# Performance work log

Measured on AMD Instinct MI355X. Metric: run time of the kernel, lower is better.

The kernel has to match this reference:

```python
import jax, jax.numpy as jnp
import numpy as np

MIN_RANGE, MAX_RANGE = 1, 3

def _build_offsets():
    # replicates TorchGrouper.__init__: offsets over a hollow cube neighborhood
    r = np.concatenate([np.arange(-MAX_RANGE, -MIN_RANGE), np.arange(MIN_RANGE, MAX_RANGE)])
    p = r.shape[0]
    rx = np.broadcast_to(r.reshape(1, 1, -1), (p, p, p))
    ry = np.broadcast_to(r.reshape(1, -1, 1), (p, p, p))
    rz = np.broadcast_to(r.reshape(-1, 1, 1), (p, p, p))
    off = np.stack([np.zeros_like(rx), rx, ry, rz], axis=3).reshape(-1, 4)  # [O,4], cols (0,x,y,z)
    return jnp.asarray(off, dtype=jnp.int32)


def setup_inputs() -> dict:
    key = jax.random.key(0)
    k1, k2, k3, k4 = jax.random.split(key, 4)
    N, Z, Y, X = 2, 40, 400, 400
    G, M, C = 40000, 100000, 64
    # voxel map values in [-1, M-1]; -1 == empty voxel (maps to zero feature row)
    voxel_maps = jax.random.randint(k1, (N, Z, Y, X), -1, M, dtype=jnp.int32)
    b = jax.random.randint(k2, (G, 1), 0, N).astype(jnp.float32)
    zyx = jax.random.uniform(k3, (G, 3), dtype=jnp.float32) * jnp.array([Z - 1, Y - 1, X - 1], jnp.float32)
    grid_positions = jnp.concatenate([b, zyx], axis=1)  # [G,4] float (batch,z,y,x)
    features = jax.random.normal(k4, (M, C), dtype=jnp.float32)
    return {"voxel_maps": voxel_maps, "grid_positions": grid_positions, "features": features}


def reference(voxel_maps, grid_positions, features):
    offsets = _build_offsets()                     # [O,4] int32
    O = offsets.shape[0]
    N, Z, Y, X = voxel_maps.shape
    G = grid_positions.shape[0]

    gp_f = grid_positions[:, None, :] + offsets[None].astype(grid_positions.dtype)  # [G,O,4] float
    gp = gp_f.astype(jnp.int32)                    # trunc-toward-zero, matches torch .long()
    bi = gp[..., 0]
    zi = jnp.clip(gp[..., 1], 0, Z - 1)
    yi = jnp.clip(gp[..., 2], 0, Y - 1)
    xi = jnp.clip(gp[..., 3], 0, X - 1)
    sampled_idx = voxel_maps[bi, zi, yi, xi]       # [G,O] int32

    feats_pad = jnp.concatenate([jnp.zeros((1, features.shape[1]), features.dtype), features], axis=0)  # [M+1,C]
    sf = feats_pad[sampled_idx + 1]                # [G,O,C]
    sampled_features = jnp.transpose(sf, (2, 0, 1))[None]  # [1,C,G,O]

    gpf = jnp.transpose(gp_f[..., 1:], (2, 0, 1))[None]    # [1,3,G,O] (z,y,x) coords
    gpf = gpf - jnp.trunc(gpf)                     # fractional part (torch .long().float())
    # faithful quirk: original adds index_offset[:, :3] == columns (0, x, y)
    gpf = gpf + offsets[:, :3].T.astype(gpf.dtype).reshape(1, 3, 1, O)

    empty_mask = jnp.sum(sampled_idx + 1, axis=1) == 0     # [G] bool
    return sampled_features, gpf, empty_mask
```

## Files before the change

### kernel.cpp

```cpp
#include <hip/hip_runtime.h>


typedef float f32x4 __attribute__((ext_vector_type(4)));

constexpr int G  = 40000;
constexpr int C  = 64;
constexpr int VZ = 40, VY = 400, VX = 400;
constexpr size_t GO = (size_t)G * 64;
constexpr int NBLK = G / 4;
constexpr int NXCD = 8;
constexpr int CHUNK = NBLK / NXCD;

__device__ __forceinline__ void store_sysnt_x4(float* p, f32x4 v) {
    asm volatile("global_store_dwordx4 %0, %1, off sc0 sc1 nt"
                 :: "v"(p), "v"(v) : "memory");
}
__device__ __forceinline__ void store_sysnt_x1(float* p, float v) {
    asm volatile("global_store_dword %0, %1, off sc0 sc1 nt"
                 :: "v"(p), "v"(v) : "memory");
}

__global__ __launch_bounds__(256) void grouper_kernel(
    const int*   __restrict__ vox,
    const float* __restrict__ gpos,
    const float* __restrict__ feat,
    float*       __restrict__ out)
{
    __shared__ __align__(16) float lds[4][64 * 32];

    const int blk = (blockIdx.x & 7) * CHUNK + (blockIdx.x >> 3);

    const int wid  = threadIdx.x >> 6;
    const int lane = threadIdx.x & 63;
    const int g = blk * 4 + wid;
    const int o = lane;

    const int rtab4[4] = {-3, -2, 1, 2};
    const int rx = rtab4[o & 3];
    const int ry = rtab4[(o >> 2) & 3];
    const int rz = rtab4[(o >> 4) & 3];

    const float4 p = ((const float4*)gpos)[g];
    const float zf = p.y + (float)rx;
    const float yf = p.z + (float)ry;
    const float xf = p.w + (float)rz;

    const int bi = (int)p.x;
    const int zi = min(max((int)zf, 0), VZ - 1);
    const int yi = min(max((int)yf, 0), VY - 1);
    const int xi = min(max((int)xf, 0), VX - 1);

    const int idx = vox[((bi * VZ + zi) * VY + yi) * VX + xi];

    float* gout = out + C * GO;
    const size_t t = (size_t)g * 64 + o;
    store_sysnt_x1(gout + t,          zf - truncf(zf));
    store_sysnt_x1(gout + GO + t,     yf - truncf(yf) + (float)rx);
    store_sysnt_x1(gout + 2 * GO + t, xf - truncf(xf) + (float)ry);
    const int allm1 = __all(idx == -1);
    if (o == 0) store_sysnt_x1(gout + 3 * GO + g, allm1 ? 1.0f : 0.0f);

    float* tile = lds[wid];
    const int d  = lane >> 3;
    const int c4 = lane & 7;
    const int q  = lane >> 4;
    const int m  = lane & 15;

    #pragma unroll
    for (int chunk = 0; chunk < 2; ++chunk) {
        #pragma unroll
        for (int i = 0; i < 8; ++i) {
            const int r    = i * 8 + d;
            const int ridx = __shfl(idx, r);
            const bool emp = ridx < 0;
            const int  rr  = emp ? 0 : ridx;
            f32x4 v = *(const f32x4*)(feat + (size_t)rr * C + chunk * 32 + c4 * 4);
            if (emp) { v.x = 0.0f; v.y = 0.0f; v.z = 0.0f; v.w = 0.0f; }
            const int cs = c4 ^ ((r >> 2) & 7);
            *(f32x4*)(tile + r * 32 + cs * 4) = v;
        }
        asm volatile("s_waitcnt lgkmcnt(0)" ::: "memory");

        #pragma unroll
        for (int i = 0; i < 8; ++i) {
            const int ip = (i ^ (m & 7)) * 4 + q;
            f32x4 sv;
            sv.x = tile[(m * 4 + 0) * 32 + ip];
            sv.y = tile[(m * 4 + 1) * 32 + ip];
            sv.z = tile[(m * 4 + 2) * 32 + ip];
            sv.w = tile[(m * 4 + 3) * 32 + ip];
            const size_t c = (size_t)(chunk * 32 + i * 4 + q);
            store_sysnt_x4(out + c * GO + (size_t)g * 64 + m * 4, sv);
        }
        asm volatile("s_waitcnt lgkmcnt(0)" ::: "memory");
    }
}

extern "C" void kernel_launch(void* const* d_in, const int* in_sizes, int n_in,
                              void* d_out, int out_size, void* d_ws, size_t ws_size,
                              hipStream_t stream) {
    const int*   vox  = (const int*)d_in[0];
    const float* gpos = (const float*)d_in[1];
    const float* feat = (const float*)d_in[2];
    float*       out  = (float*)d_out;

    grouper_kernel<<<NBLK, 256, 0, stream>>>(vox, gpos, feat, out);
}
```

Before: 194.5 us.

## Use 1024-thread blocks with per-lane row gathers and block-wide LDS transpose

Blocks now hold 16 waves (16 grid points), and each lane loads its own feature row as four 16-float pieces. A block-wide LDS transpose then lets each wave write a contiguous 4 KB run per channel instead of 256-byte runs. The XCD-aware block remapping is removed, and __syncthreads barriers across 16 waves replace the per-wave lgkmcnt waits. This adds barrier stalls and uncoalesced per-lane 64 B row reads in exchange for longer contiguous output writes.

```diff
diff --git a/kernel.cpp b/kernel.cpp
--- a/kernel.cpp
+++ b/kernel.cpp
@@ -7,9 +7,8 @@
 constexpr int C  = 64;
 constexpr int VZ = 40, VY = 400, VX = 400;
 constexpr size_t GO = (size_t)G * 64;
-constexpr int NBLK = G / 4;
-constexpr int NXCD = 8;
-constexpr int CHUNK = NBLK / NXCD;
+constexpr int GB   = 16;
+constexpr int NBLK = G / GB;
 
 __device__ __forceinline__ void store_sysnt_x4(float* p, f32x4 v) {
     asm volatile("global_store_dwordx4 %0, %1, off sc0 sc1 nt"
@@ -20,19 +19,17 @@
                  :: "v"(p), "v"(v) : "memory");
 }
 
-__global__ __launch_bounds__(256) void grouper_kernel(
+__global__ __launch_bounds__(1024, 8) void grouper_kernel(
     const int*   __restrict__ vox,
     const float* __restrict__ gpos,
     const float* __restrict__ feat,
     float*       __restrict__ out)
 {
-    __shared__ __align__(16) float lds[4][64 * 32];
+    __shared__ __align__(16) float sf[16 * 1024];
 
-    const int blk = (blockIdx.x & 7) * CHUNK + (blockIdx.x >> 3);
-
-    const int wid  = threadIdx.x >> 6;
+    const int wave = threadIdx.x >> 6;
     const int lane = threadIdx.x & 63;
-    const int g = blk * 4 + wid;
+    const int g = blockIdx.x * GB + wave;
     const int o = lane;
 
     const int rtab4[4] = {-3, -2, 1, 2};
@@ -60,39 +57,37 @@
     const int allm1 = __all(idx == -1);
     if (o == 0) store_sysnt_x1(gout + 3 * GO + g, allm1 ? 1.0f : 0.0f);
 
-    float* tile = lds[wid];
-    const int d  = lane >> 3;
-    const int c4 = lane & 7;
-    const int q  = lane >> 4;
-    const int m  = lane & 15;
+    const bool  emp = idx < 0;
+    const float* src = feat + (size_t)(emp ? 0 : idx) * C;
+    const int   base = wave * 64 + lane;
 
-    #pragma unroll
-    for (int chunk = 0; chunk < 2; ++chunk) {
+    #pragma unroll 1
+    for (int cc = 0; cc < 4; ++cc) {
+        f32x4 v0 = *(const f32x4*)(src + cc * 16 + 0);
+        f32x4 v1 = *(const f32x4*)(src + cc * 16 + 4);
+        f32x4 v2 = *(const f32x4*)(src + cc * 16 + 8);
+        f32x4 v3 = *(const f32x4*)(src + cc * 16 + 12);
+        if (emp) {
+            v0 = (f32x4)0.0f; v1 = (f32x4)0.0f; v2 = (f32x4)0.0f; v3 = (f32x4)0.0f;
+        }
+        __syncthreads();
+        sf[base +  0 * 1024] = v0.x; sf[base +  1 * 1024] = v0.y;
+        sf[base +  2 * 1024] = v0.z; sf[base +  3 * 1024] = v0.w;
+        sf[base +  4 * 1024] = v1.x; sf[base +  5 * 1024] = v1.y;
+        sf[base +  6 * 1024] = v1.z; sf[base +  7 * 1024] = v1.w;
+        sf[base +  8 * 1024] = v2.x; sf[base +  9 * 1024] = v2.y;
+        sf[base + 10 * 1024] = v2.z; sf[base + 11 * 1024] = v2.w;
+        sf[base + 12 * 1024] = v3.x; sf[base + 13 * 1024] = v3.y;
+        sf[base + 14 * 1024] = v3.z; sf[base + 15 * 1024] = v3.w;
+        __syncthreads();
+
+        const float* lsrc = sf + wave * 1024;
+        float* dst = out + (size_t)(cc * 16 + wave) * GO + (size_t)blockIdx.x * 1024;
         #pragma unroll
-        for (int i = 0; i < 8; ++i) {
-            const int r    = i * 8 + d;
-            const int ridx = __shfl(idx, r);
-            const bool emp = ridx < 0;
-            const int  rr  = emp ? 0 : ridx;
-            f32x4 v = *(const f32x4*)(feat + (size_t)rr * C + chunk * 32 + c4 * 4);
-            if (emp) { v.x = 0.0f; v.y = 0.0f; v.z = 0.0f; v.w = 0.0f; }
-            const int cs = c4 ^ ((r >> 2) & 7);
-            *(f32x4*)(tile + r * 32 + cs * 4) = v;
+        for (int j = 0; j < 4; ++j) {
+            f32x4 sv = *(const f32x4*)(lsrc + j * 256 + lane * 4);
+            store_sysnt_x4(dst + j * 256 + lane * 4, sv);
         }
-        asm volatile("s_waitcnt lgkmcnt(0)" ::: "memory");
-
-        #pragma unroll
-        for (int i = 0; i < 8; ++i) {
-            const int ip = (i ^ (m & 7)) * 4 + q;
-            f32x4 sv;
-            sv.x = tile[(m * 4 + 0) * 32 + ip];
-            sv.y = tile[(m * 4 + 1) * 32 + ip];
-            sv.z = tile[(m * 4 + 2) * 32 + ip];
-            sv.w = tile[(m * 4 + 3) * 32 + ip];
-            const size_t c = (size_t)(chunk * 32 + i * 4 + q);
-            store_sysnt_x4(out + c * GO + (size_t)g * 64 + m * 4, sv);
-        }
-        asm volatile("s_waitcnt lgkmcnt(0)" ::: "memory");
     }
 }
 
@@ -104,5 +99,5 @@
     const float* feat = (const float*)d_in[2];
     float*       out  = (float*)d_out;
 
-    grouper_kernel<<<NBLK, 256, 0, stream>>>(vox, gpos, feat, out);
+    grouper_kernel<<<NBLK, 1024, 0, stream>>>(vox, gpos, feat, out);
 }
```

Result: slower. 247.8 us (+27.4%).

## Split grouper into index pass and channel-parallel feature gather pass

Applied to the files above, without the earlier changes.

Splits the single fused kernel into two launches. The first computes voxel indices, coordinate outputs and the empty mask, and writes the indices to a workspace buffer. The second launches eight times as many blocks, each handling an 8-channel slice, and gathers features with direct strided dword stores instead of an LDS transpose. This adds a second launch, an extra round trip for the index buffer, and repeated reads of the same feature rows across channel groups. The original single kernel is kept as a fallback for when the workspace is too small.

```diff
diff --git a/kernel.cpp b/kernel.cpp
--- a/kernel.cpp
+++ b/kernel.cpp
@@ -7,32 +7,23 @@
 constexpr int C  = 64;
 constexpr int VZ = 40, VY = 400, VX = 400;
 constexpr size_t GO = (size_t)G * 64;
-constexpr int NBLK = G / 4;
-constexpr int NXCD = 8;
-constexpr int CHUNK = NBLK / NXCD;
+constexpr int NBLK1 = G / 4;
+constexpr int NBLK2 = 8 * (G / 4);
 
-__device__ __forceinline__ void store_sysnt_x4(float* p, f32x4 v) {
-    asm volatile("global_store_dwordx4 %0, %1, off sc0 sc1 nt"
-                 :: "v"(p), "v"(v) : "memory");
-}
 __device__ __forceinline__ void store_sysnt_x1(float* p, float v) {
     asm volatile("global_store_dword %0, %1, off sc0 sc1 nt"
                  :: "v"(p), "v"(v) : "memory");
 }
 
-__global__ __launch_bounds__(256) void grouper_kernel(
+__global__ __launch_bounds__(256) void pass1_kernel(
     const int*   __restrict__ vox,
     const float* __restrict__ gpos,
-    const float* __restrict__ feat,
-    float*       __restrict__ out)
+    float*       __restrict__ out,
+    int*         __restrict__ idxbuf)
 {
-    __shared__ __align__(16) float lds[4][64 * 32];
-
-    const int blk = (blockIdx.x & 7) * CHUNK + (blockIdx.x >> 3);
-
     const int wid  = threadIdx.x >> 6;
     const int lane = threadIdx.x & 63;
-    const int g = blk * 4 + wid;
+    const int g = blockIdx.x * 4 + wid;
     const int o = lane;
 
     const int rtab4[4] = {-3, -2, 1, 2};
@@ -52,6 +43,79 @@
 
     const int idx = vox[((bi * VZ + zi) * VY + yi) * VX + xi];
 
+    const size_t t = (size_t)g * 64 + o;
+    asm volatile("global_store_dword %0, %1, off sc0 sc1 nt"
+                 :: "v"(idxbuf + t), "v"(idx) : "memory");
+
+    float* gout = out + C * GO;
+    store_sysnt_x1(gout + t,          zf - truncf(zf));
+    store_sysnt_x1(gout + GO + t,     yf - truncf(yf) + (float)rx);
+    store_sysnt_x1(gout + 2 * GO + t, xf - truncf(xf) + (float)ry);
+    const int allm1 = __all(idx == -1);
+    if (o == 0) store_sysnt_x1(gout + 3 * GO + g, allm1 ? 1.0f : 0.0f);
+}
+
+__global__ __launch_bounds__(256) void pass2_kernel(
+    const float* __restrict__ feat,
+    const int*   __restrict__ idxbuf,
+    float*       __restrict__ out)
+{
+    const int cg   = blockIdx.x & 7;
+    const int tile = blockIdx.x >> 3;
+    const int wid  = threadIdx.x >> 6;
+    const int lane = threadIdx.x & 63;
+    const int g = tile * 4 + wid;
+
+    const size_t t = (size_t)g * 64 + lane;
+    const int row = __builtin_nontemporal_load(idxbuf + t);
+    const bool emp = row < 0;
+
+    const float* fp = feat + (size_t)(emp ? 0 : row) * C + cg * 8;
+    f32x4 v0 = *(const f32x4*)fp;
+    f32x4 v1 = *(const f32x4*)(fp + 4);
+    if (emp) { v0 = (f32x4)0.0f; v1 = (f32x4)0.0f; }
+
+    float* dst = out + (size_t)(cg * 8) * GO + t;
+    store_sysnt_x1(dst + 0 * GO, v0.x);
+    store_sysnt_x1(dst + 1 * GO, v0.y);
+    store_sysnt_x1(dst + 2 * GO, v0.z);
+    store_sysnt_x1(dst + 3 * GO, v0.w);
+    store_sysnt_x1(dst + 4 * GO, v1.x);
+    store_sysnt_x1(dst + 5 * GO, v1.y);
+    store_sysnt_x1(dst + 6 * GO, v1.z);
+    store_sysnt_x1(dst + 7 * GO, v1.w);
+}
+
+__device__ __forceinline__ void store_sysnt_x4(float* p, f32x4 v) {
+    asm volatile("global_store_dwordx4 %0, %1, off sc0 sc1 nt"
+                 :: "v"(p), "v"(v) : "memory");
+}
+
+__global__ __launch_bounds__(256) void grouper_single(
+    const int*   __restrict__ vox,
+    const float* __restrict__ gpos,
+    const float* __restrict__ feat,
+    float*       __restrict__ out)
+{
+    __shared__ __align__(16) float lds[4][64 * 32];
+    const int blk = (blockIdx.x & 7) * (NBLK1 / 8) + (blockIdx.x >> 3);
+    const int wid  = threadIdx.x >> 6;
+    const int lane = threadIdx.x & 63;
+    const int g = blk * 4 + wid;
+    const int o = lane;
+    const int rtab4[4] = {-3, -2, 1, 2};
+    const int rx = rtab4[o & 3];
+    const int ry = rtab4[(o >> 2) & 3];
+    const int rz = rtab4[(o >> 4) & 3];
+    const float4 p = ((const float4*)gpos)[g];
+    const float zf = p.y + (float)rx;
+    const float yf = p.z + (float)ry;
+    const float xf = p.w + (float)rz;
+    const int bi = (int)p.x;
+    const int zi = min(max((int)zf, 0), VZ - 1);
+    const int yi = min(max((int)yf, 0), VY - 1);
+    const int xi = min(max((int)xf, 0), VX - 1);
+    const int idx = vox[((bi * VZ + zi) * VY + yi) * VX + xi];
     float* gout = out + C * GO;
     const size_t t = (size_t)g * 64 + o;
     store_sysnt_x1(gout + t,          zf - truncf(zf));
@@ -59,13 +123,11 @@
     store_sysnt_x1(gout + 2 * GO + t, xf - truncf(xf) + (float)ry);
     const int allm1 = __all(idx == -1);
     if (o == 0) store_sysnt_x1(gout + 3 * GO + g, allm1 ? 1.0f : 0.0f);
-
     float* tile = lds[wid];
     const int d  = lane >> 3;
     const int c4 = lane & 7;
     const int q  = lane >> 4;
     const int m  = lane & 15;
-
     #pragma unroll
     for (int chunk = 0; chunk < 2; ++chunk) {
         #pragma unroll
@@ -80,7 +142,6 @@
             *(f32x4*)(tile + r * 32 + cs * 4) = v;
         }
         asm volatile("s_waitcnt lgkmcnt(0)" ::: "memory");
-
         #pragma unroll
         for (int i = 0; i < 8; ++i) {
             const int ip = (i ^ (m & 7)) * 4 + q;
@@ -104,5 +165,12 @@
     const float* feat = (const float*)d_in[2];
     float*       out  = (float*)d_out;
 
-    grouper_kernel<<<NBLK, 256, 0, stream>>>(vox, gpos, feat, out);
+    const size_t need = (size_t)G * 64 * sizeof(int);
+    if (ws_size >= need) {
+        int* idxbuf = (int*)d_ws;
+        pass1_kernel<<<NBLK1, 256, 0, stream>>>(vox, gpos, out, idxbuf);
+        pass2_kernel<<<NBLK2, 256, 0, stream>>>(feat, idxbuf, out);
+    } else {
+        grouper_single<<<NBLK1, 256, 0, stream>>>(vox, gpos, feat, out);
+    }
 }
```

New measurement: 380.7 us. +95.7%, slower.
